# Performance work log

Measured on AMD Instinct MI355X. Metric: run time of the kernel, lower is better.

The kernel has to match this reference:

```python
import jax, jax.numpy as jnp
import numpy as np

N, L, C, K = 8, 6400, 256, 100  # batch, tokens per image (80x80), feat dim, n_topics
EPS = 1e-12  # F.normalize eps


def _l1_normalize(x):
    return x / jnp.maximum(jnp.sum(jnp.abs(x), axis=-1, keepdims=True), EPS)


def setup_inputs() -> dict:
    key = jax.random.key(0)
    k1, k2, k3 = jax.random.split(key, 3)
    feat = jax.random.normal(k1, (N, L, C), dtype=jnp.float32)
    prob_topics = jax.random.uniform(k2, (N, 2 * L, K), dtype=jnp.float32)
    # topics are hard (0/1) topic assignments per token
    topics = (jax.random.uniform(k3, (N, 2 * L, K)) > 0.5).astype(jnp.float32)
    return {"feat": feat, "prob_topics": prob_topics, "topics": topics, "n_samples": 8}


def reference(feat, prob_topics, topics, n_samples):
    n, l, c = feat.shape
    # ---- sample_topic (eval path: top-k over mixed topic distribution) ----
    p0, p1 = prob_topics[:, :l], prob_topics[:, l:]
    t0 = topics[:, :l]
    theta0 = _l1_normalize(jnp.sum(p0, axis=1))           # [N, K]
    theta1 = _l1_normalize(jnp.sum(p1, axis=1))           # [N, K]
    theta = _l1_normalize(theta0 * theta1)                # [N, K]
    _, sampled_inds = jax.lax.top_k(theta, n_samples)     # [N, n_samples]
    # gather topic columns for every token: [N, L, n_samples]
    sampled_topics0 = jnp.take_along_axis(t0, sampled_inds[:, None, :], axis=-1)
    topick = sampled_topics0[..., 0]                      # [N, L] binary membership of top topic

    # ---- reduce_feat: ragged boolean gather -> left-packed padded buffer ----
    # (padded to L, the static upper bound, for jit-compatible shapes)
    mask = topick > 0.5                                   # [N, L] selected tokens
    len_topic = jnp.sum(topick, axis=-1).astype(jnp.int32)  # [N]
    rank = jnp.cumsum(topick, axis=1).astype(jnp.int32) - 1  # dest slot per selected token
    dest = jnp.where(mask, rank, l)                       # unselected -> overflow slot l
    rows = jnp.arange(n)[:, None]                         # [N, 1]
    vals = jnp.where(mask[..., None], feat, 0.0)          # [N, L, C]
    resized_feat = jnp.zeros((n, l + 1, c), dtype=feat.dtype).at[rows, dest].set(vals)[:, :l]
    new_mask = jnp.arange(l)[None, :] < len_topic[:, None]  # [N, L] valid-slot mask
    return resized_feat, new_mask
```

## Files before the change

kernel.cpp:

```cpp
#include <hip/hip_runtime.h>

#define N 8
#define L 6400
#define C 256
#define K 100
#define CPS 32
#define RPC (L / CPS)

__global__ void kA_partial(const float* __restrict__ prob, double* __restrict__ P) {
    int b = blockIdx.x;
    int seg = b >> 5, chunk = b & 31;
    int t = threadIdx.x;
    int r8 = t >> 5, g = t & 31;
    const float4* base = (const float4*)prob
        + (size_t)seg * (L * 25) + (size_t)chunk * (RPC * 25);
    double a0 = 0, a1 = 0, a2 = 0, a3 = 0;
    if (g < 25) {
#pragma unroll
        for (int i = 0; i < RPC / 8; ++i) {
            float4 v = base[(i * 8 + r8) * 25 + g];
            a0 += v.x; a1 += v.y; a2 += v.z; a3 += v.w;
        }
    }
    __shared__ double sdata[8][100];
    if (g < 25) {
        int k4 = g * 4;
        sdata[r8][k4] = a0; sdata[r8][k4 + 1] = a1;
        sdata[r8][k4 + 2] = a2; sdata[r8][k4 + 3] = a3;
    }
    __syncthreads();
    if (t < 100) {
        double s = 0;
#pragma unroll
        for (int r = 0; r < 8; ++r) s += sdata[r][t];
        P[b * 100 + t] = s;
    }
}

__global__ void kB_argmax(const double* __restrict__ P, int* __restrict__ kstar) {
    int n = blockIdx.x, t = threadIdx.x;
    __shared__ double vbuf[100];
    if (t < 100) {
        const double* p0 = P + (size_t)(2 * n) * CPS * 100 + t;
        const double* p1 = P + (size_t)(2 * n + 1) * CPS * 100 + t;
        double s0 = 0, s1 = 0;
#pragma unroll 8
        for (int c = 0; c < CPS; ++c) { s0 += p0[c * 100]; s1 += p1[c * 100]; }
        vbuf[t] = s0 * s1;
    }
    __syncthreads();
    if (t == 0) {
        double best = -1.0; int bi = 0;
        for (int k = 0; k < K; ++k) {
            double v = vbuf[k];
            if (v > best) { best = v; bi = k; }
        }
        kstar[n] = bi;
    }
}

__global__ void kC_bits(const float* __restrict__ topics,
                        const int* __restrict__ kstar,
                        unsigned long long* __restrict__ bits) {
    int idx = blockIdx.x * 256 + threadIdx.x;
    int n = idx / L;
    int l = idx - n * L;
    int k = kstar[n];
    float v = topics[((size_t)n * 2 * L + (size_t)l) * K + (size_t)k];
    unsigned long long bal = __ballot(v > 0.5f);
    if ((threadIdx.x & 63) == 0) bits[idx >> 6] = bal;
}

__global__ void kD_scan(const unsigned long long* __restrict__ bits,
                        int* __restrict__ woffs, int* __restrict__ lenbuf,
                        float* __restrict__ out) {
    int n = blockIdx.x, t = threadIdx.x;
    __shared__ int cnts[100];
    __shared__ int len_s;
    if (t < 100) cnts[t] = __popcll(bits[n * 100 + t]);
    __syncthreads();
    if (t < 100) {
        int s = 0;
        for (int w = 0; w < t; ++w) s += cnts[w];
        woffs[n * 100 + t] = s;
    }
    if (t == 0) {
        int s = 0;
        for (int w = 0; w < 100; ++w) s += cnts[w];
        lenbuf[n] = s; len_s = s;
    }
    __syncthreads();
    int len = len_s;
    float* om = out + (size_t)N * L * C + (size_t)n * L;
    for (int idx = t; idx < L; idx += 128) om[idx] = (idx < len) ? 1.0f : 0.0f;
}

__global__ void __launch_bounds__(256)
kE_out(const float* __restrict__ feat,
       const unsigned long long* __restrict__ bits,
       const int* __restrict__ woffs, const int* __restrict__ lenbuf,
       float* __restrict__ out) {
    int r = blockIdx.x * 4 + (threadIdx.x >> 6);
    int lane = threadIdx.x & 63;
    int n = r / L;
    int l = r - n * L;
    unsigned long long word = bits[r >> 6];
    int len = lenbuf[n];
    const float4* f4 = (const float4*)feat;
    float4* o4 = (float4*)out;
    int bpos = l & 63;
    if ((word >> bpos) & 1ull) {
        int d = woffs[n * 100 + (l >> 6)]
              + __popcll(word & ((1ull << bpos) - 1ull));
        float4 v = f4[(size_t)r * 64 + lane];
        o4[((size_t)n * L + (size_t)d) * 64 + lane] = v;
    }
    if (l >= len)
        o4[(size_t)r * 64 + lane] = make_float4(0.f, 0.f, 0.f, 0.f);
}

extern "C" void kernel_launch(void* const* d_in, const int* in_sizes, int n_in,
                              void* d_out, int out_size, void* d_ws, size_t ws_size,
                              hipStream_t stream) {
    const float* feat   = (const float*)d_in[0];
    const float* prob   = (const float*)d_in[1];
    const float* topics = (const float*)d_in[2];

    double* P                 = (double*)d_ws;
    unsigned long long* bits  = (unsigned long long*)(P + 512 * 100);
    int* woffs                = (int*)(bits + 800);
    int* kstar                = woffs + 800;
    int* lenbuf               = kstar + 8;

    float* out = (float*)d_out;

    kA_partial<<<16 * CPS, 256, 0, stream>>>(prob, P);
    kB_argmax <<<N, 128, 0, stream>>>(P, kstar);
    kC_bits   <<<(N * L) / 256, 256, 0, stream>>>(topics, kstar, bits);
    kD_scan   <<<N, 128, 0, stream>>>(bits, woffs, lenbuf, out);
    kE_out    <<<(N * L) / 4, 256, 0, stream>>>(feat, bits, woffs, lenbuf, out);
}
```

Measured before the change: 172.6 us.

## Fuse argmax with bit extraction and scan with packing to cut launches

Merges the argmax kernel into the ballot-bit kernel, so each of the 200 blocks recomputes the top topic redundantly from the partial sums. Merges the prefix-scan and mask write into the packing kernel: each of 800 blocks redoes a 100-word shared-memory scan, then copies 64 rows with 16 rows per wavefront. The aim is to remove two kernel launches and their dependency gaps, in exchange for redundant argmax and scan work in every block and fewer, larger blocks for the copy.

```diff
diff --git a/kernel.cpp b/kernel.cpp
--- a/kernel.cpp
+++ b/kernel.cpp
@@ -37,9 +37,13 @@
     }
 }
 
-__global__ void kB_argmax(const double* __restrict__ P, int* __restrict__ kstar) {
-    int n = blockIdx.x, t = threadIdx.x;
+__global__ void __launch_bounds__(256)
+kBC(const double* __restrict__ P, const float* __restrict__ topics,
+    unsigned long long* __restrict__ bits) {
+    int b = blockIdx.x, t = threadIdx.x;
+    int n = b / 25, blk = b - n * 25;
     __shared__ double vbuf[100];
+    __shared__ int ks_s;
     if (t < 100) {
         const double* p0 = P + (size_t)(2 * n) * CPS * 100 + t;
         const double* p1 = P + (size_t)(2 * n + 1) * CPS * 100 + t;
@@ -55,68 +59,58 @@
             double v = vbuf[k];
             if (v > best) { best = v; bi = k; }
         }
-        kstar[n] = bi;
+        ks_s = bi;
     }
-}
-
-__global__ void kC_bits(const float* __restrict__ topics,
-                        const int* __restrict__ kstar,
-                        unsigned long long* __restrict__ bits) {
-    int idx = blockIdx.x * 256 + threadIdx.x;
-    int n = idx / L;
-    int l = idx - n * L;
-    int k = kstar[n];
+    __syncthreads();
+    int k = ks_s;
+    int l = blk * 256 + t;
     float v = topics[((size_t)n * 2 * L + (size_t)l) * K + (size_t)k];
     unsigned long long bal = __ballot(v > 0.5f);
-    if ((threadIdx.x & 63) == 0) bits[idx >> 6] = bal;
-}
-
-__global__ void kD_scan(const unsigned long long* __restrict__ bits,
-                        int* __restrict__ woffs, int* __restrict__ lenbuf,
-                        float* __restrict__ out) {
-    int n = blockIdx.x, t = threadIdx.x;
-    __shared__ int cnts[100];
-    __shared__ int len_s;
-    if (t < 100) cnts[t] = __popcll(bits[n * 100 + t]);
-    __syncthreads();
-    if (t < 100) {
-        int s = 0;
-        for (int w = 0; w < t; ++w) s += cnts[w];
-        woffs[n * 100 + t] = s;
-    }
-    if (t == 0) {
-        int s = 0;
-        for (int w = 0; w < 100; ++w) s += cnts[w];
-        lenbuf[n] = s; len_s = s;
-    }
-    __syncthreads();
-    int len = len_s;
-    float* om = out + (size_t)N * L * C + (size_t)n * L;
-    for (int idx = t; idx < L; idx += 128) om[idx] = (idx < len) ? 1.0f : 0.0f;
+    if ((t & 63) == 0) bits[n * 100 + (l >> 6)] = bal;
 }
 
 __global__ void __launch_bounds__(256)
-kE_out(const float* __restrict__ feat,
-       const unsigned long long* __restrict__ bits,
-       const int* __restrict__ woffs, const int* __restrict__ lenbuf,
-       float* __restrict__ out) {
-    int r = blockIdx.x * 4 + (threadIdx.x >> 6);
-    int lane = threadIdx.x & 63;
-    int n = r / L;
-    int l = r - n * L;
-    unsigned long long word = bits[r >> 6];
-    int len = lenbuf[n];
+kDE(const float* __restrict__ feat, const unsigned long long* __restrict__ bits,
+    float* __restrict__ out) {
+    int b = blockIdx.x, t = threadIdx.x;
+    int n = b / 100, w = b - n * 100;
+    __shared__ unsigned long long sb[100];
+    __shared__ int sA[128], sB[128];
+    if (t < 100) sb[t] = bits[n * 100 + t];
+    __syncthreads();
+    int c = (t < 100) ? __popcll(sb[t]) : 0;
+    if (t < 128) sA[t] = c;
+    __syncthreads();
+    int* src = sA; int* dst = sB;
+    for (int off = 1; off < 128; off <<= 1) {
+        if (t < 128) dst[t] = src[t] + ((t >= off) ? src[t - off] : 0);
+        __syncthreads();
+        int* tmp = src; src = dst; dst = tmp;
+    }
+    int len = src[127];
+    int pre = (w > 0) ? src[w - 1] : 0;
+    unsigned long long word = sb[w];
+
     const float4* f4 = (const float4*)feat;
     float4* o4 = (float4*)out;
-    int bpos = l & 63;
-    if ((word >> bpos) & 1ull) {
-        int d = woffs[n * 100 + (l >> 6)]
-              + __popcll(word & ((1ull << bpos) - 1ull));
-        float4 v = f4[(size_t)r * 64 + lane];
-        o4[((size_t)n * L + (size_t)d) * 64 + lane] = v;
+    int lane = t & 63, wv = t >> 6;
+#pragma unroll 4
+    for (int j = 0; j < 16; ++j) {
+        int li = wv * 16 + j;
+        int l = w * 64 + li;
+        size_t r = (size_t)n * L + l;
+        if ((word >> li) & 1ull) {
+            int d = pre + __popcll(word & ((1ull << li) - 1ull));
+            float4 v = f4[r * 64 + lane];
+            o4[((size_t)n * L + (size_t)d) * 64 + lane] = v;
+        }
+        if (l >= len)
+            o4[r * 64 + lane] = make_float4(0.f, 0.f, 0.f, 0.f);
     }
-    if (l >= len)
-        o4[(size_t)r * 64 + lane] = make_float4(0.f, 0.f, 0.f, 0.f);
+    if (t < 64) {
+        int l = w * 64 + t;
+        out[(size_t)N * L * C + (size_t)n * L + l] = (l < len) ? 1.0f : 0.0f;
+    }
 }
 
 extern "C" void kernel_launch(void* const* d_in, const int* in_sizes, int n_in,
@@ -126,17 +120,12 @@
     const float* prob   = (const float*)d_in[1];
     const float* topics = (const float*)d_in[2];
 
-    double* P                 = (double*)d_ws;
-    unsigned long long* bits  = (unsigned long long*)(P + 512 * 100);
-    int* woffs                = (int*)(bits + 800);
-    int* kstar                = woffs + 800;
-    int* lenbuf               = kstar + 8;
+    double* P                = (double*)d_ws;
+    unsigned long long* bits = (unsigned long long*)(P + 512 * 100);
 
     float* out = (float*)d_out;
 
     kA_partial<<<16 * CPS, 256, 0, stream>>>(prob, P);
-    kB_argmax <<<N, 128, 0, stream>>>(P, kstar);
-    kC_bits   <<<(N * L) / 256, 256, 0, stream>>>(topics, kstar, bits);
-    kD_scan   <<<N, 128, 0, stream>>>(bits, woffs, lenbuf, out);
-    kE_out    <<<(N * L) / 4, 256, 0, stream>>>(feat, bits, woffs, lenbuf, out);
+    kBC       <<<N * 25, 256, 0, stream>>>(P, topics, bits);
+    kDE       <<<N * 100, 256, 0, stream>>>(feat, bits, out);
 }
```

Result: no change. 170.9 us (-1.0%).
